# Optimization experiments

Hardware: AMD Instinct MI355X
Metric: run time of the kernel (lower is better)

## Reference

```python
import jax, jax.numpy as jnp
import numpy as np

K = 500        # conv kernel == stride (non-overlapping windows)
C_IN = 8       # embedding dim
C_OUT = 128    # conv out channels
VOCAB = 257    # 256 byte values + padding idx 256


def setup_inputs() -> dict:
    key = jax.random.key(0)
    ks = jax.random.split(key, 10)
    B, L = 8, 1 << 20
    x = jax.random.randint(ks[0], (B, L), 0, VOCAB, dtype=jnp.int32)
    emb = 0.1 * jax.random.normal(ks[1], (VOCAB, C_IN), jnp.float32)
    emb = emb.at[VOCAB - 1].set(0.0)  # padding_idx=256 -> zero row
    lim_c = 1.0 / np.sqrt(C_IN * K)
    w1 = jax.random.uniform(ks[2], (C_OUT, C_IN, K), jnp.float32, -lim_c, lim_c)
    b1 = jax.random.uniform(ks[3], (C_OUT,), jnp.float32, -lim_c, lim_c)
    w2 = jax.random.uniform(ks[4], (C_OUT, C_IN, K), jnp.float32, -lim_c, lim_c)
    b2 = jax.random.uniform(ks[5], (C_OUT,), jnp.float32, -lim_c, lim_c)
    lim_d = 1.0 / np.sqrt(C_OUT)
    wd1 = jax.random.uniform(ks[6], (C_OUT, C_OUT), jnp.float32, -lim_d, lim_d)
    bd1 = jax.random.uniform(ks[7], (C_OUT,), jnp.float32, -lim_d, lim_d)
    wd2 = jax.random.uniform(ks[8], (1, C_OUT), jnp.float32, -lim_d, lim_d)
    bd2 = jax.random.uniform(ks[9], (1,), jnp.float32, -lim_d, lim_d)
    return {"x": x, "emb": emb, "w1": w1, "b1": b1, "w2": w2, "b2": b2,
            "wd1": wd1, "bd1": bd1, "wd2": wd2, "bd2": bd2}


def reference(x, emb, w1, b1, w2, b2, wd1, bd1, wd2, bd2):
    B, L = x.shape
    T = (L - K) // K + 1  # valid conv output length (== L // K here)
    xe = emb[x]                                  # [B, L, 8]  embedding lookup
    win = xe[:, : T * K].reshape(B, T, K, C_IN)  # [B, T, 500, 8] non-overlap windows
    c1 = jnp.einsum('btke,oek->bto', win, w1) + b1  # [B, T, 128]
    c2 = jnp.einsum('btke,oek->bto', win, w2) + b2
    gated = jax.nn.relu(c1) * jax.nn.sigmoid(c2)    # gated activation
    pooled = jnp.max(gated, axis=1)                 # global max pool over time -> [B, 128]
    h = jax.nn.relu(pooled @ wd1.T + bd1)           # [B, 128]
    out = jax.nn.sigmoid(h @ wd2.T + bd2)           # [B, 1]
    return out
```

## Files before the change

kernel.cpp:

```cpp
#include <hip/hip_runtime.h>

#define BATCH   8
#define LSEQ    1048576
#define KCONV   500
#define TWIN    2097
#define MROWS   16776
#define KDIM    4000
#define NDIM    256
#define COUT    128
#define VOCAB   257
#define VOCABP  256

#define BMR     80
#define NTILE   210
#define SLABP   20
#define NSLAB   25
#define NG      125
#define PLANE   (NDIM * 32)
#define AROWSH  168
#define STAGEN  (BMR * SLABP)
#define TSTRIDE 18

#define WTF_OFF   0ull
#define WTF_BYTES ((size_t)NG * PLANE * 2)
#define POOL_OFF  (WTF_OFF + WTF_BYTES)
#define CNT_OFF   (POOL_OFF + 4096)

typedef __attribute__((ext_vector_type(8))) __bf16 bf16x8;
typedef __attribute__((ext_vector_type(4))) float  floatx4;

__device__ inline unsigned short f2bf(float f) {
    union { float f; unsigned u; } c; c.f = f;
    return (unsigned short)((c.u + 0x7FFFu + ((c.u >> 16) & 1u)) >> 16);
}
__device__ inline unsigned pack2(float lo, float hi) {
    return (unsigned)f2bf(lo) | ((unsigned)f2bf(hi) << 16);
}

#define LDS_BARRIER() asm volatile("s_waitcnt lgkmcnt(0)\n\ts_barrier" ::: "memory")

__global__ __launch_bounds__(256) void wprep_kernel(const float* __restrict__ w1,
                                                    const float* __restrict__ w2,
                                                    unsigned short* __restrict__ Wtf,
                                                    float* __restrict__ pool,
                                                    int* __restrict__ cnt) {
    const int n   = blockIdx.x;
    const int tid = threadIdx.x;
    __shared__ float tile[KDIM];
    const float* src = (n < COUT) ? (w1 + (size_t)n * KDIM)
                                  : (w2 + (size_t)(n - COUT) * KDIM);
    for (int i = tid; i < KDIM; i += 256) tile[i] = src[i];
    __syncthreads();
    for (int i = tid; i < KDIM; i += 256) {
        int g = i >> 5, kk = i & 31;
        Wtf[(size_t)g * PLANE + n * 32 + kk] = f2bf(tile[(i & 7) * KCONV + (i >> 3)]);
    }
    if (n == 0) {
        if (tid < 256) ((float4*)pool)[tid] = float4{0.f, 0.f, 0.f, 0.f};
        if (tid == 0) *cnt = 0;
    }
}

__global__ __launch_bounds__(512) void gemm_kernel(const int* __restrict__ x,
                                                   const float* __restrict__ emb,
                                                   const unsigned short* __restrict__ Wtf,
                                                   const float* __restrict__ b1,
                                                   const float* __restrict__ b2,
                                                   float* __restrict__ pool,
                                                   int* __restrict__ cnt,
                                                   const float* __restrict__ wd1,
                                                   const float* __restrict__ bd1,
                                                   const float* __restrict__ wd2,
                                                   const float* __restrict__ bd2,
                                                   float* __restrict__ out) {
    __shared__ __align__(16) unsigned short tableL[VOCAB * TSTRIDE];
    __shared__ __align__(16) unsigned short As[2][BMR * AROWSH];

    const int tid  = threadIdx.x;
    const int lane = tid & 63;
    const int wv   = tid >> 6;
    const int m0   = blockIdx.x * BMR;
    const int r16  = lane & 15;
    const int q    = lane >> 4;

    if (tid < VOCAB) {
        const float4* er = (const float4*)(emb + tid * 8);
        float4 a = er[0], b = er[1];
        unsigned* tb = (unsigned*)(tableL + tid * TSTRIDE);
        tb[0] = pack2(a.x, a.y); tb[1] = pack2(a.z, a.w);
        tb[2] = pack2(b.x, b.y); tb[3] = pack2(b.z, b.w);
    }

    const int* xptr[4];
    int        loff[4];
    bool       sval[4];
    bool       sact[4];
#pragma unroll
    for (int l = 0; l < 4; ++l) {
        sact[l] = (l < 3) || (tid < STAGEN - 3 * 512);
        int idx = tid + 512 * l;
        sval[l] = (idx < STAGEN);
        int ic  = sval[l] ? idx : 0;
        int row = ic / SLABP;
        int pos = ic - row * SLABP;
        int am  = m0 + row;
        bool av = sval[l] && (am < MROWS);
        sval[l] = av;
        int amc = av ? am : 0;
        int b   = amc / TWIN;
        int t   = amc - b * TWIN;
        xptr[l] = x + ((size_t)b * LSEQ + (size_t)t * KCONV + pos);
        loff[l] = row * AROWSH + pos * 8;
    }

    const int o = wv * 16 + r16;
    const size_t boff0 = (size_t)o * 32 + q * 8;
    const size_t boff1 = (size_t)(o + 128) * 32 + q * 8;

    floatx4 acc[5][2];
#pragma unroll
    for (int i = 0; i < 5; ++i) { acc[i][0] = floatx4{0,0,0,0}; acc[i][1] = floatx4{0,0,0,0}; }

    int xv[4], xn[4];
#pragma unroll
    for (int l = 0; l < 4; ++l) xv[l] = sval[l] ? xptr[l][0] : VOCABP;
    __syncthreads();

#pragma unroll
    for (int l = 0; l < 4; ++l) {
        if (sact[l]) {
            const unsigned* gb = (const unsigned*)(tableL + xv[l] * TSTRIDE);
            uint4 g; g.x = gb[0]; g.y = gb[1]; g.z = gb[2]; g.w = gb[3];
            *(uint4*)((unsigned short*)As + loff[l]) = g;
        }
    }
#pragma unroll
    for (int l = 0; l < 4; ++l) xv[l] = sval[l] ? xptr[l][SLABP] : VOCABP;
    LDS_BARRIER();

    bf16x8 bc0[2], bc1[2], bc2[2] = {};
    bc0[0] = *(const bf16x8*)(Wtf + boff0);
    bc0[1] = *(const bf16x8*)(Wtf + boff1);
    bc1[0] = *(const bf16x8*)(Wtf + PLANE + boff0);
    bc1[1] = *(const bf16x8*)(Wtf + PLANE + boff1);

    int buf = 0;
    for (int s = 0; s < NSLAB; ++s) {
        if (s + 2 < NSLAB) {
#pragma unroll
            for (int l = 0; l < 4; ++l)
                xn[l] = sval[l] ? xptr[l][(s + 2) * SLABP] : VOCABP;
        }

        const unsigned short* Asb  = (const unsigned short*)As + buf * (BMR * AROWSH);
        unsigned short*       dstS = (unsigned short*)As + (buf ^ 1) * (BMR * AROWSH);
        const bool stg = (s + 1 < NSLAB);
        uint4 gr[4];

#pragma unroll
        for (int kt = 0; kt < 5; ++kt) {
            const int g = s * 5 + kt;
            if (g + 2 < NG) {
                const unsigned short* Wp = Wtf + (size_t)(g + 2) * PLANE;
                bc2[0] = *(const bf16x8*)(Wp + boff0);
                bc2[1] = *(const bf16x8*)(Wp + boff1);
            }
            bf16x8 af[5];
#pragma unroll
            for (int i = 0; i < 5; ++i)
                af[i] = *(const bf16x8*)(Asb + (i * 16 + r16) * AROWSH + (kt * 4 + q) * 8);

            if (kt < 4 && stg && sact[kt]) {
                const unsigned* gb = (const unsigned*)(tableL + xv[kt] * TSTRIDE);
                gr[kt].x = gb[0]; gr[kt].y = gb[1]; gr[kt].z = gb[2]; gr[kt].w = gb[3];
            }

#pragma unroll
            for (int i = 0; i < 5; ++i) {
                acc[i][0] = __builtin_amdgcn_mfma_f32_16x16x32_bf16(af[i], bc0[0], acc[i][0], 0, 0, 0);
                acc[i][1] = __builtin_amdgcn_mfma_f32_16x16x32_bf16(af[i], bc0[1], acc[i][1], 0, 0, 0);
            }
            bc0[0] = bc1[0]; bc0[1] = bc1[1];
            bc1[0] = bc2[0]; bc1[1] = bc2[1];

            if (kt >= 1 && stg && sact[kt - 1])
                *(uint4*)(dstS + loff[kt - 1]) = gr[kt - 1];
        }
#pragma unroll
        for (int l = 0; l < 4; ++l) xv[l] = xn[l];
        LDS_BARRIER();
        buf ^= 1;
    }

    const float b1v = b1[o], b2v = b2[o];
    float cur = 0.0f;
    int curb  = (m0 + q * 4) / TWIN;
#pragma unroll
    for (int i = 0; i < 5; ++i) {
#pragma unroll
        for (int rg = 0; rg < 4; ++rg) {
            const int row = m0 + i * 16 + q * 4 + rg;
            if (row < MROWS) {
                const int bb = row / TWIN;
                if (bb != curb) {
                    atomicMax((int*)&pool[curb * COUT + o], __float_as_int(cur));
                    cur = 0.0f; curb = bb;
                }
                const float c1 = acc[i][0][rg] + b1v;
                const float c2 = acc[i][1][rg] + b2v;
                const float g  = fmaxf(c1, 0.0f) / (1.0f + __expf(-c2));
                cur = fmaxf(cur, g);
            }
        }
    }
    atomicMax((int*)&pool[curb * COUT + o], __float_as_int(cur));

    asm volatile("s_waitcnt vmcnt(0)" ::: "memory");
    __syncthreads();
    __shared__ int lastFlag;
    if (tid == 0) {
        int prev = __hip_atomic_fetch_add(cnt, 1, __ATOMIC_RELAXED, __HIP_MEMORY_SCOPE_AGENT);
        lastFlag = (prev == NTILE - 1) ? 1 : 0;
    }
    __syncthreads();
    if (!lastFlag) return;

    float* poolL = (float*)As;
    float* red   = poolL + BATCH * COUT;
    poolL[tid] = __int_as_float(
        __hip_atomic_load((int*)&pool[tid], __ATOMIC_RELAXED, __HIP_MEMORY_SCOPE_AGENT));
    poolL[tid + 512] = __int_as_float(
        __hip_atomic_load((int*)&pool[tid + 512], __ATOMIC_RELAXED, __HIP_MEMORY_SCOPE_AGENT));
    __syncthreads();

    if (tid < COUT) {
        const int j = tid;
        const float wj = wd2[j];
#pragma unroll
        for (int b = 0; b < BATCH; ++b) {
            float s = bd1[j];
            for (int i = 0; i < COUT; ++i) s += poolL[b * COUT + i] * wd1[j * COUT + i];
            red[b * COUT + j] = fmaxf(s, 0.0f) * wj;
        }
    }
    __syncthreads();
    if (tid < BATCH) {
        float s = 0.0f;
        for (int i = 0; i < COUT; ++i) s += red[tid * COUT + i];
        out[tid] = 1.0f / (1.0f + expf(-(s + bd2[0])));
    }
}

extern "C" void kernel_launch(void* const* d_in, const int* in_sizes, int n_in,
                              void* d_out, int out_size, void* d_ws, size_t ws_size,
                              hipStream_t stream) {
    const int*   x   = (const int*)d_in[0];
    const float* emb = (const float*)d_in[1];
    const float* w1  = (const float*)d_in[2];
    const float* b1  = (const float*)d_in[3];
    const float* w2  = (const float*)d_in[4];
    const float* b2  = (const float*)d_in[5];
    const float* wd1 = (const float*)d_in[6];
    const float* bd1 = (const float*)d_in[7];
    const float* wd2 = (const float*)d_in[8];
    const float* bd2 = (const float*)d_in[9];
    float* out = (float*)d_out;

    unsigned short* Wtf  = (unsigned short*)((char*)d_ws + WTF_OFF);
    float*          pool = (float*)((char*)d_ws + POOL_OFF);
    int*            cnt  = (int*)((char*)d_ws + CNT_OFF);

    wprep_kernel<<<dim3(NDIM), dim3(256), 0, stream>>>(w1, w2, Wtf, pool, cnt);
    gemm_kernel<<<dim3(NTILE), dim3(512), 0, stream>>>(x, emb, Wtf, b1, b2, pool, cnt,
                                                       wd1, bd1, wd2, bd2, out);
}
```

Baseline: 161.1 us.

## Fuse weight prep into GEMM kernel with cooperative grid sync

Merges the weight transpose/bf16 conversion kernel into the main GEMM kernel, launched cooperatively. Each thread converts one (output channel, k-group) chunk using vectorized float4 reads, then a grid-wide sync ensures the converted weights are visible before the MMA loop. This removes one kernel launch and the gap between the two kernels, and overlaps weight prep with the embedding table and first A-slab staging. The cost is a grid barrier and a dependence on all 210 blocks being co-resident.

```diff
diff --git a/kernel.cpp b/kernel.cpp
--- a/kernel.cpp
+++ b/kernel.cpp
@@ -1,4 +1,7 @@
 #include <hip/hip_runtime.h>
+#include <hip/hip_cooperative_groups.h>
+
+namespace cg = cooperative_groups;
 
 #define BATCH   8
 #define LSEQ    1048576
@@ -39,40 +42,20 @@
 
 #define LDS_BARRIER() asm volatile("s_waitcnt lgkmcnt(0)\n\ts_barrier" ::: "memory")
 
-__global__ __launch_bounds__(256) void wprep_kernel(const float* __restrict__ w1,
+__global__ __launch_bounds__(512) void fused_kernel(const int* __restrict__ x,
+                                                    const float* __restrict__ emb,
+                                                    const float* __restrict__ w1,
                                                     const float* __restrict__ w2,
+                                                    const float* __restrict__ b1,
+                                                    const float* __restrict__ b2,
                                                     unsigned short* __restrict__ Wtf,
                                                     float* __restrict__ pool,
-                                                    int* __restrict__ cnt) {
-    const int n   = blockIdx.x;
-    const int tid = threadIdx.x;
-    __shared__ float tile[KDIM];
-    const float* src = (n < COUT) ? (w1 + (size_t)n * KDIM)
-                                  : (w2 + (size_t)(n - COUT) * KDIM);
-    for (int i = tid; i < KDIM; i += 256) tile[i] = src[i];
-    __syncthreads();
-    for (int i = tid; i < KDIM; i += 256) {
-        int g = i >> 5, kk = i & 31;
-        Wtf[(size_t)g * PLANE + n * 32 + kk] = f2bf(tile[(i & 7) * KCONV + (i >> 3)]);
-    }
-    if (n == 0) {
-        if (tid < 256) ((float4*)pool)[tid] = float4{0.f, 0.f, 0.f, 0.f};
-        if (tid == 0) *cnt = 0;
-    }
-}
-
-__global__ __launch_bounds__(512) void gemm_kernel(const int* __restrict__ x,
-                                                   const float* __restrict__ emb,
-                                                   const unsigned short* __restrict__ Wtf,
-                                                   const float* __restrict__ b1,
-                                                   const float* __restrict__ b2,
-                                                   float* __restrict__ pool,
-                                                   int* __restrict__ cnt,
-                                                   const float* __restrict__ wd1,
-                                                   const float* __restrict__ bd1,
-                                                   const float* __restrict__ wd2,
-                                                   const float* __restrict__ bd2,
-                                                   float* __restrict__ out) {
+                                                    int* __restrict__ cnt,
+                                                    const float* __restrict__ wd1,
+                                                    const float* __restrict__ bd1,
+                                                    const float* __restrict__ wd2,
+                                                    const float* __restrict__ bd2,
+                                                    float* __restrict__ out) {
     __shared__ __align__(16) unsigned short tableL[VOCAB * TSTRIDE];
     __shared__ __align__(16) unsigned short As[2][BMR * AROWSH];
 
@@ -82,6 +65,30 @@
     const int m0   = blockIdx.x * BMR;
     const int r16  = lane & 15;
     const int q    = lane >> 4;
+
+    {
+        const int gtid = blockIdx.x * 512 + tid;
+        if (gtid < NDIM * NG) {
+            const int n = gtid / NG;
+            const int g = gtid - n * NG;
+            const float* src = (n < COUT) ? (w1 + (size_t)n * KDIM)
+                                          : (w2 + (size_t)(n - COUT) * KDIM);
+            unsigned short o16[32];
+#pragma unroll
+            for (int e = 0; e < 8; ++e) {
+                float4 v = *(const float4*)(src + e * KCONV + g * 4);
+                o16[e +  0] = f2bf(v.x);
+                o16[e +  8] = f2bf(v.y);
+                o16[e + 16] = f2bf(v.z);
+                o16[e + 24] = f2bf(v.w);
+            }
+            uint4* dst = (uint4*)(Wtf + (size_t)g * PLANE + n * 32);
+            const uint4* s4 = (const uint4*)o16;
+            dst[0] = s4[0]; dst[1] = s4[1]; dst[2] = s4[2]; dst[3] = s4[3];
+        }
+        if (gtid < 256) ((float4*)pool)[gtid] = float4{0.f, 0.f, 0.f, 0.f};
+        if (gtid == 0) *cnt = 0;
+    }
 
     if (tid < VOCAB) {
         const float4* er = (const float4*)(emb + tid * 8);
@@ -138,6 +145,8 @@
     for (int l = 0; l < 4; ++l) xv[l] = sval[l] ? xptr[l][SLABP] : VOCABP;
     LDS_BARRIER();
 
+    cg::this_grid().sync();
+
     bf16x8 bc0[2], bc1[2], bc2[2] = {};
     bc0[0] = *(const bf16x8*)(Wtf + boff0);
     bc0[1] = *(const bf16x8*)(Wtf + boff1);
@@ -270,7 +279,10 @@
     float*          pool = (float*)((char*)d_ws + POOL_OFF);
     int*            cnt  = (int*)((char*)d_ws + CNT_OFF);
 
-    wprep_kernel<<<dim3(NDIM), dim3(256), 0, stream>>>(w1, w2, Wtf, pool, cnt);
-    gemm_kernel<<<dim3(NTILE), dim3(512), 0, stream>>>(x, emb, Wtf, b1, b2, pool, cnt,
-                                                       wd1, bd1, wd2, bd2, out);
-}
+    void* args[] = { (void*)&x, (void*)&emb, (void*)&w1, (void*)&w2,
+                     (void*)&b1, (void*)&b2, (void*)&Wtf, (void*)&pool,
+                     (void*)&cnt, (void*)&wd1, (void*)&bd1, (void*)&wd2,
+                     (void*)&bd2, (void*)&out };
+    hipLaunchCooperativeKernel((const void*)fused_kernel, dim3(NTILE), dim3(512),
+                               args, 0, stream);
+}
```

After: 205.4 us. 27.6% more time.
